# Kernel optimization log

Hardware: AMD Instinct MI355X
Metric: run time of the kernel (lower is better)

## Reference

```python
import jax, jax.numpy as jnp
import numpy as np

N, E, CN, CE = 2048, 8192, 256, 256
MN, ME = 16384, 65536
RATIO = 0.5
K_KEEP = int(np.ceil(RATIO * N))  # 1024, static


def _glorot(key, shape):
    lim = float(np.sqrt(6.0 / (shape[0] + shape[1])))
    return jax.random.uniform(key, shape, jnp.float32, -lim, lim)


def setup_inputs() -> dict:
    key = jax.random.key(0)
    ks = jax.random.split(key, 16)
    return {
        "x_n": jax.random.normal(ks[0], (N, CN), jnp.float32),
        "edge_index_n": jax.random.randint(ks[1], (2, MN), 0, N),
        "edge_weight_n": jax.random.uniform(ks[2], (MN,), jnp.float32),
        "x_e": jax.random.normal(ks[3], (E, CE), jnp.float32),
        "edge_index_e": jax.random.randint(ks[4], (2, ME), 0, E),
        "edge_weight_e": jax.random.uniform(ks[5], (ME,), jnp.float32),
        "edge_index": jax.random.randint(ks[6], (2, E), 0, N),
        "n_batch": jnp.zeros((N,), jnp.int64 if jax.config.jax_enable_x64 else jnp.int32),
        "e_batch": jnp.zeros((E,), jnp.int64 if jax.config.jax_enable_x64 else jnp.int32),
        "x_n0": jax.random.normal(ks[7], (N, CN), jnp.float32),
        "x_e0": jax.random.normal(ks[8], (E, CE), jnp.float32),
        # HodgeLaguerreConv(in, 1, K=2) params for node- and edge-scoring GNNs
        "W_n0": _glorot(ks[9], (CN, 1)),
        "W_n1": _glorot(ks[10], (CN, 1)),
        "b_n": jnp.zeros((1,), jnp.float32),
        "W_e0": _glorot(ks[11], (CE, 1)),
        "W_e1": _glorot(ks[12], (CE, 1)),
        "b_e": jnp.zeros((1,), jnp.float32),
    }


def _hodge_conv_k2(x, ei, ew, W0, W1, b):
    # PyG: out = lin0(T0) + lin1(T1), T0 = x, T1 = x - L@x (propagate: dst += w_e * x[src])
    n = x.shape[0]
    agg = jax.ops.segment_sum(ew[:, None] * x[ei[0]], ei[1], num_segments=n)
    return x @ W0 + (x - agg) @ W1 + b


def reference(x_n, edge_index_n, edge_weight_n, x_e, edge_index_e, edge_weight_e,
              edge_index, n_batch, e_batch, x_n0, x_e0,
              W_n0, W_n1, b_n, W_e0, W_e1, b_e):
    score_n = jax.nn.sigmoid(_hodge_conv_k2(x_n, edge_index_n, edge_weight_n, W_n0, W_n1, b_n).reshape(-1))
    score_e = jax.nn.sigmoid(_hodge_conv_k2(x_e, edge_index_e, edge_weight_e, W_e0, W_e1, b_e).reshape(-1))
    xns = x_n * score_n[:, None]
    xes = x_e * score_e[:, None]
    # incidence matrix B (par1): B[src,e]=-1, B[dst,e]=+1 (duplicates summed, as torch sparse)
    src, dst = edge_index[0], edge_index[1]
    eidx = jnp.arange(E)
    par1 = jnp.zeros((N, E), x_n.dtype).at[src, eidx].add(-1.0).at[dst, eidx].add(1.0)
    par1_abs = jnp.zeros((N, E), x_n.dtype).at[src, eidx].add(1.0).at[dst, eidx].add(1.0)
    # joint node score with 0.125 * |B| @ score_e
    joint = score_n + 0.125 * (par1_abs @ score_e)
    perm = jnp.argsort(-joint)                # descending
    idx_keep = jnp.sort(perm[:K_KEEP])        # kept nodes in original order (boolean-mask order)
    mask_n = jnp.zeros((N,), x_n.dtype).at[idx_keep].set(1.0)
    # edges touching any removed node get nonzero; keep edges where this is exactly 0
    removed_hits = par1_abs.T @ (1.0 - mask_n)
    keep_e = (removed_hits == 0.0).astype(x_n.dtype)     # [E]
    # masked incidence: kept-node rows, removed-edge columns zeroed
    par_masked = par1[idx_keep] * keep_e[None, :]        # [k, E]
    L0 = par_masked @ par_masked.T                       # [k, k]  (equals compacted L0)
    L1 = par_masked.T @ par_masked                       # [E, E]  (zero rows/cols at removed edges)
    # eigsh(L0, k=1, 'LM'): max eigenvalue; scipy path is non-differentiable -> stop_gradient
    lam = jax.lax.stop_gradient(jnp.linalg.eigvalsh(L0)[-1])
    L0s = 2.0 * L0 / lam
    L1s = 2.0 * L1 / lam
    x_n_out = xns[idx_keep]
    x_e_out = xes * keep_e[:, None]
    x_n0_out = x_n0[idx_keep]
    x_e0_out = x_e0 * keep_e[:, None]
    return (x_n_out, L0s, x_e_out, L1s, par_masked, x_n0_out, x_e0_out)
```

## Files before the change

kernel.cpp:

```cpp
#include <hip/hip_runtime.h>
#include <math.h>

#define NN   2048
#define EE   8192
#define CNF  256
#define MN   16384
#define ME   65536
#define KK   1024

#define OUT_XN   ((size_t)0)
#define OUT_L0   ((size_t)262144)
#define OUT_XE   ((size_t)1310720)
#define OUT_L1   ((size_t)3407872)
#define OUT_PM   ((size_t)70516736)
#define OUT_XN0  ((size_t)78905344)
#define OUT_XE0  ((size_t)79167488)

#define WS_T1N    0
#define WS_SLINN  2048
#define WS_T1E    4096
#define WS_SLINE  12288
#define WS_SCN    20480
#define WS_SCE    22528
#define WS_AGGN   32768
#define WS_AGGE   34816
#define WS_LAM    43008
#define WS_IDXK   43520
#define WS_RANK   44544
#define WS_OFFS   47616
#define WS_ADJE   66176
#define WS_KEEPE  82560

#define DCAP  8
#define PWR_T 64
#define RBAD  0xFFFFu

typedef float vf4 __attribute__((ext_vector_type(4)));

__global__ void k_prep(const float* __restrict__ xn, const float* __restrict__ xe,
                       const float* __restrict__ Wn0, const float* __restrict__ Wn1,
                       const float* __restrict__ We0, const float* __restrict__ We1,
                       float* __restrict__ wsf) {
    if (blockIdx.x == 0) {
        for (int i = threadIdx.x; i < 2048; i += 256) wsf[WS_AGGN + i] = 0.f;
        for (int i = threadIdx.x; i < 8192; i += 256) wsf[WS_AGGE + i] = 0.f;
    }
    int gw = (blockIdx.x * blockDim.x + threadIdx.x) >> 6;
    int lane = threadIdx.x & 63;
    int wstr = (gridDim.x * blockDim.x) >> 6;
    for (int row = gw; row < NN + EE; row += wstr) {
        const float *x, *W0, *W1; float *t1, *sl; int r;
        if (row < NN) { r = row;      x = xn + (size_t)r * CNF; W0 = Wn0; W1 = Wn1; t1 = wsf + WS_T1N; sl = wsf + WS_SLINN; }
        else          { r = row - NN; x = xe + (size_t)r * CNF; W0 = We0; W1 = We1; t1 = wsf + WS_T1E; sl = wsf + WS_SLINE; }
        float4 xv = ((const float4*)x)[lane];
        float4 w0 = ((const float4*)W0)[lane];
        float4 w1 = ((const float4*)W1)[lane];
        float d0 = xv.x*w0.x + xv.y*w0.y + xv.z*w0.z + xv.w*w0.w;
        float d1 = xv.x*w1.x + xv.y*w1.y + xv.z*w1.z + xv.w*w1.w;
        #pragma unroll
        for (int o = 32; o > 0; o >>= 1) { d0 += __shfl_down(d0, o, 64); d1 += __shfl_down(d1, o, 64); }
        if (lane == 0) { t1[r] = d1; sl[r] = d0 + d1; }
    }
}

__global__ void k_agg(const int* __restrict__ ein, const float* __restrict__ ewn,
                      const int* __restrict__ eie, const float* __restrict__ ewe,
                      float* __restrict__ wsf) {
    int i = blockIdx.x * blockDim.x + threadIdx.x;
    if (i < MN) {
        int s = ein[i], d = ein[MN + i];
        atomicAdd(wsf + WS_AGGN + d, ewn[i] * wsf[WS_T1N + s]);
    }
    if (i < ME) {
        int s = eie[i], d = eie[ME + i];
        atomicAdd(wsf + WS_AGGE + d, ewe[i] * wsf[WS_T1E + s]);
    }
}

__device__ __forceinline__ float block_reduce_sum(float val, float* red) {
    #pragma unroll
    for (int o = 32; o > 0; o >>= 1) val += __shfl_down(val, o, 64);
    int lane = threadIdx.x & 63, wid = threadIdx.x >> 6;
    if (lane == 0) red[wid] = val;
    __syncthreads();
    float r = 0.0f;
    if (threadIdx.x < 16) {
        r = red[threadIdx.x];
        #pragma unroll
        for (int o = 8; o > 0; o >>= 1) r += __shfl_down(r, o, 16);
        if (threadIdx.x == 0) red[0] = r;
    }
    __syncthreads();
    float out = red[0];
    __syncthreads();
    return out;
}

__global__ __launch_bounds__(1024) void k_mid(
        const int* __restrict__ ei,
        const float* __restrict__ bn, const float* __restrict__ be,
        float* __restrict__ out, float* __restrict__ wsf, int* __restrict__ wsi) {
    int tid = threadIdx.x;
    if (blockIdx.x != 0) {
        size_t w = (size_t)(blockIdx.x - 1) * 1024 + tid;
        size_t ws = (size_t)(gridDim.x - 1) * 1024;
        vf4 z = (vf4)(0.0f);
        vf4* l1 = (vf4*)(out + OUT_L1);
        for (size_t p = w; p < (size_t)EE * EE / 4; p += ws) __builtin_nontemporal_store(z, &l1[p]);
        vf4* pm = (vf4*)(out + OUT_PM);
        for (size_t p = w; p < (size_t)KK * EE / 4; p += ws) __builtin_nontemporal_store(z, &pm[p]);
        vf4* l0 = (vf4*)(out + OUT_L0);
        for (size_t p = w; p < (size_t)KK * KK / 4; p += ws) __builtin_nontemporal_store(z, &l0[p]);
        return;
    }
    __shared__ unsigned long long s_u64[2048];
    __shared__ float s_joint[2048];
    __shared__ unsigned short s_rank[2048];
    __shared__ unsigned short s_adjo[16384 + DCAP];
    __shared__ float s_red[16];
    int* s_i = (int*)s_u64;

    float bnv = bn[0], bev = be[0];
    for (int i = tid; i < NN; i += 1024) {
        float zv = wsf[WS_SLINN + i] - wsf[WS_AGGN + i] + bnv;
        float s = 1.0f / (1.0f + expf(-zv));
        wsf[WS_SCN + i] = s;
        s_joint[i] = s;
    }
    for (int j = tid; j < EE; j += 1024) {
        float zv = wsf[WS_SLINE + j] - wsf[WS_AGGE + j] + bev;
        wsf[WS_SCE + j] = 1.0f / (1.0f + expf(-zv));
    }
    __syncthreads();

    for (int e = tid; e < EE; e += 1024) {
        float v = 0.125f * wsf[WS_SCE + e];
        atomicAdd(&s_joint[ei[e]], v);
        atomicAdd(&s_joint[ei[EE + e]], v);
    }
    __syncthreads();

    for (int i = tid; i < 2048; i += 1024) {
        float f = s_joint[i];
        unsigned u = __float_as_uint(f);
        unsigned sk = (u & 0x80000000u) ? ~u : (u | 0x80000000u);
        s_u64[i] = (((unsigned long long)(~sk)) << 32) | (unsigned)i;
    }
    __syncthreads();
    for (int k = 2; k <= 2048; k <<= 1) {
        for (int j = k >> 1; j >= 1; j >>= 1) {
            for (int i = tid; i < 2048; i += 1024) {
                int ixj = i ^ j;
                if (ixj > i) {
                    bool up = ((i & k) == 0);
                    unsigned long long a = s_u64[i], b = s_u64[ixj];
                    if ((a > b) == up) { s_u64[i] = b; s_u64[ixj] = a; }
                }
            }
            __syncthreads();
        }
    }
    int myid = (int)(s_u64[tid] & 0xFFFFFFFFu);
    __syncthreads();
    {
        s_i[tid] = 0; s_i[tid + 1024] = 0; s_i[tid + 2048] = 0;
        __syncthreads();
        s_i[myid] = 1;
        __syncthreads();
        int a0 = s_i[2 * tid], a1 = s_i[2 * tid + 1];
        int pairsum = a0 + a1;
        s_i[2048 + tid] = pairsum;
        __syncthreads();
        for (int off = 1; off < 1024; off <<= 1) {
            int v = (tid >= off) ? s_i[2048 + tid - off] : 0;
            __syncthreads();
            s_i[2048 + tid] += v;
            __syncthreads();
        }
        int excl = s_i[2048 + tid] - pairsum;
        int i0 = 2 * tid, i1 = 2 * tid + 1;
        int r0 = excl, r1 = excl + a0;
        s_rank[i0] = a0 ? (unsigned short)r0 : (unsigned short)RBAD;
        s_rank[i1] = a1 ? (unsigned short)r1 : (unsigned short)RBAD;
        wsi[WS_RANK + i0] = a0 ? r0 : -1;
        wsi[WS_RANK + i1] = a1 ? r1 : -1;
        if (a0) wsi[WS_IDXK + r0] = i0;
        if (a1) wsi[WS_IDXK + r1] = i1;
    }
    __syncthreads();

    s_i[tid] = 0;
    __syncthreads();
    for (int e = tid; e < EE; e += 1024) {
        int s = ei[e], d = ei[EE + e];
        unsigned rs = s_rank[s], rd = s_rank[d];
        int kept = (rs != RBAD && rd != RBAD);
        wsi[WS_KEEPE + e] = kept;
        if (kept && s != d) {
            atomicAdd(&s_i[(int)rs], 1);
            atomicAdd(&s_i[(int)rd], 1);
        }
    }
    __syncthreads();

    {
        int dg = s_i[tid];
        s_i[1024 + tid] = dg;
        for (int off = 1; off < 1024; off <<= 1) {
            __syncthreads();
            int v = (tid >= off) ? s_i[1024 + tid - off] : 0;
            __syncthreads();
            s_i[1024 + tid] += v;
        }
        __syncthreads();
        int offs = s_i[1024 + tid] - dg;
        s_i[2048 + tid] = offs;
        wsi[WS_OFFS + tid] = offs;
        if (tid == 1023) wsi[WS_OFFS + 1024] = s_i[1024 + 1023];
    }
    __syncthreads();

    for (int e = tid; e < EE; e += 1024) {
        int s = ei[e], d = ei[EE + e];
        unsigned rs = s_rank[s], rd = s_rank[d];
        if (rs != RBAD && rd != RBAD && s != d) {
            int p = atomicAdd(&s_i[2048 + (int)rs], 1);
            s_adjo[p] = (unsigned short)rd;
            wsi[WS_ADJE + p] = (e << 1);
            int q = atomicAdd(&s_i[2048 + (int)rd], 1);
            s_adjo[q] = (unsigned short)rs;
            wsi[WS_ADJE + q] = (e << 1) | 1;
        }
    }
    __syncthreads();

    {
        int o0 = wsi[WS_OFFS + tid];
        int d  = wsi[WS_OFFS + tid + 1] - o0;
        __syncthreads();
        float* v0 = (float*)s_u64;
        float* v1 = v0 + 1024;
        unsigned h = (unsigned)tid * 2654435761u + 911u;
        h ^= h >> 15; h *= 2246822519u; h ^= h >> 13;
        v0[tid] = (float)(h & 0xFFFFu) * (1.0f / 65536.0f) - 0.5f;
        int aj[DCAP];
        #pragma unroll
        for (int j = 0; j < DCAP; ++j) aj[j] = (j < d) ? (int)s_adjo[o0 + j] : 0;
        __syncthreads();
        float* vc = v0; float* vn = v1;
        for (int iter = 0; iter < PWR_T; ++iter) {
            float acc = 0.0f;
            #pragma unroll
            for (int j = 0; j < DCAP; ++j) acc += (j < d) ? vc[aj[j]] : 0.0f;
            for (int i = o0 + DCAP; i < o0 + d; ++i) acc += vc[(int)s_adjo[i]];
            float y = (float)d * vc[tid] - acc;
            if ((iter & 7) == 7) {
                float n2 = block_reduce_sum(y * y, s_red);
                y *= (n2 > 0.0f) ? rsqrtf(n2) : 0.0f;
            }
            vn[tid] = y;
            __syncthreads();
            float* tmp = vc; vc = vn; vn = tmp;
        }
        float acc = 0.0f;
        #pragma unroll
        for (int j = 0; j < DCAP; ++j) acc += (j < d) ? vc[aj[j]] : 0.0f;
        for (int i = o0 + DCAP; i < o0 + d; ++i) acc += vc[(int)s_adjo[i]];
        float y = (float)d * vc[tid] - acc;
        float rq = block_reduce_sum(vc[tid] * y, s_red);
        if (tid == 0) wsf[WS_LAM] = rq;
    }
}

__global__ __launch_bounds__(1024) void k_final(
        const float* __restrict__ xn, const float* __restrict__ xe,
        const float* __restrict__ xn0, const float* __restrict__ xe0,
        const int* __restrict__ ei,
        float* __restrict__ out, const float* __restrict__ wsf,
        const int* __restrict__ wsi) {
    float sc = 2.0f / wsf[WS_LAM];
    int gt = blockIdx.x * 1024 + threadIdx.x;
    int gstr = gridDim.x * 1024;

    for (int i = gt; i < KK * 64; i += gstr) {
        int r = i >> 6, c = i & 63;
        int src = wsi[WS_IDXK + r];
        float s = wsf[WS_SCN + src];
        float4 v = ((const float4*)(xn + (size_t)src * CNF))[c];
        v.x *= s; v.y *= s; v.z *= s; v.w *= s;
        ((float4*)(out + OUT_XN))[(size_t)r * 64 + c] = v;
        ((float4*)(out + OUT_XN0))[(size_t)r * 64 + c] = ((const float4*)(xn0 + (size_t)src * CNF))[c];
    }
    for (int i = gt; i < EE * 64; i += gstr) {
        int e = i >> 6, c = i & 63;
        float m = wsi[WS_KEEPE + e] ? 1.0f : 0.0f;
        float s = m * wsf[WS_SCE + e];
        float4 v = ((const float4*)(xe + (size_t)e * CNF))[c];
        v.x *= s; v.y *= s; v.z *= s; v.w *= s;
        ((float4*)(out + OUT_XE))[(size_t)e * 64 + c] = v;
        float4 v0 = ((const float4*)(xe0 + (size_t)e * CNF))[c];
        v0.x *= m; v0.y *= m; v0.z *= m; v0.w *= m;
        ((float4*)(out + OUT_XE0))[(size_t)e * 64 + c] = v0;
    }
    {
        float* pm = out + OUT_PM;
        float* L0 = out + OUT_L0;
        for (int e = gt; e < EE; e += gstr) {
            int s = ei[e], d = ei[EE + e];
            int rs = wsi[WS_RANK + s], rd = wsi[WS_RANK + d];
            if (rs < 0 || rd < 0 || s == d) continue;
            pm[(size_t)rs * EE + e] = -1.0f;
            pm[(size_t)rd * EE + e] =  1.0f;
            atomicAdd(&L0[(size_t)rs * KK + rs],  sc);
            atomicAdd(&L0[(size_t)rd * KK + rd],  sc);
            atomicAdd(&L0[(size_t)rs * KK + rd], -sc);
            atomicAdd(&L0[(size_t)rd * KK + rs], -sc);
        }
    }
    {
        float* L1 = out + OUT_L1;
        int gwv = gt >> 6, lane = gt & 63, wstr = gstr >> 6;
        for (int r = gwv; r < KK; r += wstr) {
            int o0 = wsi[WS_OFFS + r], o1 = wsi[WS_OFFS + r + 1];
            for (int i = o0; i < o1; ++i) {
                int eiv = wsi[WS_ADJE + i];
                int e = eiv >> 1;
                float si = (eiv & 1) ? sc : -sc;
                for (int j = o0 + lane; j < o1; j += 64) {
                    int ejv = wsi[WS_ADJE + j];
                    atomicAdd(&L1[(size_t)e * EE + (ejv >> 1)], (ejv & 1) ? si : -si);
                }
            }
        }
    }
}

extern "C" void kernel_launch(void* const* d_in, const int* in_sizes, int n_in,
                              void* d_out, int out_size, void* d_ws, size_t ws_size,
                              hipStream_t stream) {
    const float* x_n  = (const float*)d_in[0];
    const int*   ei_n = (const int*)  d_in[1];
    const float* ew_n = (const float*)d_in[2];
    const float* x_e  = (const float*)d_in[3];
    const int*   ei_e = (const int*)  d_in[4];
    const float* ew_e = (const float*)d_in[5];
    const int*   ei   = (const int*)  d_in[6];
    const float* x_n0 = (const float*)d_in[9];
    const float* x_e0 = (const float*)d_in[10];
    const float* Wn0  = (const float*)d_in[11];
    const float* Wn1  = (const float*)d_in[12];
    const float* bn   = (const float*)d_in[13];
    const float* We0  = (const float*)d_in[14];
    const float* We1  = (const float*)d_in[15];
    const float* be   = (const float*)d_in[16];

    float* out = (float*)d_out;
    float* wsf = (float*)d_ws;
    int*   wsi = (int*)d_ws;

    k_prep <<<640, 256, 0, stream>>>(x_n, x_e, Wn0, Wn1, We0, We1, wsf);
    k_agg  <<<256, 256, 0, stream>>>(ei_n, ew_n, ei_e, ew_e, wsf);
    k_mid  <<<256, 1024, 0, stream>>>(ei, bn, be, out, wsf, wsi);
    k_final<<<256, 1024, 0, stream>>>(x_n, x_e, x_n0, x_e0, ei, out, wsf, wsi);
}
```

Before: 472.6 us.

## Replace bitonic sort with radix select, wave-scan, and single-wave power iteration

Replaces the 2048-element bitonic sort used for top-K with a 6-pass 8-bit radix select that finds the K-th key threshold, then ranks kept nodes with a shuffle-based block scan. The Hillis-Steele shared-memory scans are swapped for a wave-shuffle scan. The power iteration now runs on a single 64-lane wavefront that handles 16 nodes per lane, so it needs no block barriers, and normalisation is deferred into the next iteration. The aim is to remove the many __syncthreads in this serial block, at the cost of less parallelism in the power iteration. The Rayleigh quotient is now divided by the last norm, and tie-breaking changes to index-reversed keys.

Result: slower. 1.150 ms (+143.4%).

```diff
diff --git a/kernel.cpp b/kernel.cpp
--- a/kernel.cpp
+++ b/kernel.cpp
@@ -77,23 +77,28 @@
     }
 }
 
-__device__ __forceinline__ float block_reduce_sum(float val, float* red) {
+__device__ __forceinline__ int block_incl_scan_1024(int v, int* t16) {
+    int lane = threadIdx.x & 63, wid = threadIdx.x >> 6;
+    int x = v;
     #pragma unroll
-    for (int o = 32; o > 0; o >>= 1) val += __shfl_down(val, o, 64);
-    int lane = threadIdx.x & 63, wid = threadIdx.x >> 6;
-    if (lane == 0) red[wid] = val;
-    __syncthreads();
-    float r = 0.0f;
+    for (int o = 1; o < 64; o <<= 1) {
+        int t = __shfl_up(x, o, 64);
+        if (lane >= o) x += t;
+    }
+    if (lane == 63) t16[wid] = x;
+    __syncthreads();
     if (threadIdx.x < 16) {
-        r = red[threadIdx.x];
-        #pragma unroll
-        for (int o = 8; o > 0; o >>= 1) r += __shfl_down(r, o, 16);
-        if (threadIdx.x == 0) red[0] = r;
-    }
-    __syncthreads();
-    float out = red[0];
-    __syncthreads();
-    return out;
+        int w = t16[threadIdx.x];
+        #pragma unroll
+        for (int o = 1; o < 16; o <<= 1) {
+            int t = __shfl_up(w, o, 16);
+            if ((int)threadIdx.x >= o) w += t;
+        }
+        t16[threadIdx.x] = w;
+    }
+    __syncthreads();
+    int base = wid ? t16[wid - 1] : 0;
+    return base + x;
 }
 
 __global__ __launch_bounds__(1024) void k_mid(
@@ -117,7 +122,7 @@
     __shared__ float s_joint[2048];
     __shared__ unsigned short s_rank[2048];
     __shared__ unsigned short s_adjo[16384 + DCAP];
-    __shared__ float s_red[16];
+    __shared__ int s_t16[16];
     int* s_i = (int*)s_u64;
 
     float bnv = bn[0], bev = be[0];
@@ -140,44 +145,59 @@
     }
     __syncthreads();
 
-    for (int i = tid; i < 2048; i += 1024) {
-        float f = s_joint[i];
-        unsigned u = __float_as_uint(f);
-        unsigned sk = (u & 0x80000000u) ? ~u : (u | 0x80000000u);
-        s_u64[i] = (((unsigned long long)(~sk)) << 32) | (unsigned)i;
-    }
-    __syncthreads();
-    for (int k = 2; k <= 2048; k <<= 1) {
-        for (int j = k >> 1; j >= 1; j >>= 1) {
-            for (int i = tid; i < 2048; i += 1024) {
-                int ixj = i ^ j;
-                if (ixj > i) {
-                    bool up = ((i & k) == 0);
-                    unsigned long long a = s_u64[i], b = s_u64[ixj];
-                    if ((a > b) == up) { s_u64[i] = b; s_u64[ixj] = a; }
-                }
+    unsigned long long k0, k1;
+    {
+        int i0 = 2 * tid, i1 = 2 * tid + 1;
+        float f0 = s_joint[i0], f1 = s_joint[i1];
+        unsigned u0 = __float_as_uint(f0), u1 = __float_as_uint(f1);
+        unsigned sk0 = (u0 & 0x80000000u) ? ~u0 : (u0 | 0x80000000u);
+        unsigned sk1 = (u1 & 0x80000000u) ? ~u1 : (u1 | 0x80000000u);
+        k0 = (((unsigned long long)sk0) << 11) | (unsigned long long)(2047 - i0);
+        k1 = (((unsigned long long)sk1) << 11) | (unsigned long long)(2047 - i1);
+    }
+    unsigned long long prefix = 0ULL;
+    int rem = KK;
+    #pragma unroll
+    for (int p = 5; p >= 0; --p) {
+        __syncthreads();
+        if (tid < 256) s_i[tid] = 0;
+        __syncthreads();
+        int sh = p << 3;
+        unsigned long long ph = prefix >> (sh + 8);
+        if ((k0 >> (sh + 8)) == ph) atomicAdd(&s_i[(int)((k0 >> sh) & 255)], 1);
+        if ((k1 >> (sh + 8)) == ph) atomicAdd(&s_i[(int)((k1 >> sh) & 255)], 1);
+        __syncthreads();
+        if (tid < 64) {
+            int b0 = s_i[4 * tid + 0], b1 = s_i[4 * tid + 1];
+            int b2 = s_i[4 * tid + 2], b3 = s_i[4 * tid + 3];
+            int sl = b0 + b1 + b2 + b3;
+            int si = sl;
+            #pragma unroll
+            for (int o = 1; o < 64; o <<= 1) {
+                int t = __shfl_down(si, o, 64);
+                if (tid + o < 64) si += t;
             }
-            __syncthreads();
-        }
-    }
-    int myid = (int)(s_u64[tid] & 0xFFFFFFFFu);
-    __syncthreads();
-    {
-        s_i[tid] = 0; s_i[tid + 1024] = 0; s_i[tid + 2048] = 0;
+            int sup = si - sl;
+            int sg3 = sup;
+            int sg2 = sg3 + b3;
+            int sg1 = sg2 + b2;
+            int sg0 = sg1 + b1;
+            if (sg0 < rem && rem <= sg0 + b0) { s_i[256] = (tid << 2) | 0; s_i[257] = rem - sg0; }
+            if (sg1 < rem && rem <= sg1 + b1) { s_i[256] = (tid << 2) | 1; s_i[257] = rem - sg1; }
+            if (sg2 < rem && rem <= sg2 + b2) { s_i[256] = (tid << 2) | 2; s_i[257] = rem - sg2; }
+            if (sg3 < rem && rem <= sg3 + b3) { s_i[256] = (tid << 2) | 3; s_i[257] = rem - sg3; }
+        }
         __syncthreads();
-        s_i[myid] = 1;
+        prefix |= ((unsigned long long)(unsigned)s_i[256]) << sh;
+        rem = s_i[257];
+    }
+    {
+        int a0 = (k0 >= prefix) ? 1 : 0;
+        int a1 = (k1 >= prefix) ? 1 : 0;
+        int pr = a0 + a1;
         __syncthreads();
-        int a0 = s_i[2 * tid], a1 = s_i[2 * tid + 1];
-        int pairsum = a0 + a1;
-        s_i[2048 + tid] = pairsum;
-        __syncthreads();
-        for (int off = 1; off < 1024; off <<= 1) {
-            int v = (tid >= off) ? s_i[2048 + tid - off] : 0;
-            __syncthreads();
-            s_i[2048 + tid] += v;
-            __syncthreads();
-        }
-        int excl = s_i[2048 + tid] - pairsum;
+        int incl = block_incl_scan_1024(pr, s_t16);
+        int excl = incl - pr;
         int i0 = 2 * tid, i1 = 2 * tid + 1;
         int r0 = excl, r1 = excl + a0;
         s_rank[i0] = a0 ? (unsigned short)r0 : (unsigned short)RBAD;
@@ -205,18 +225,11 @@
 
     {
         int dg = s_i[tid];
-        s_i[1024 + tid] = dg;
-        for (int off = 1; off < 1024; off <<= 1) {
-            __syncthreads();
-            int v = (tid >= off) ? s_i[1024 + tid - off] : 0;
-            __syncthreads();
-            s_i[1024 + tid] += v;
-        }
-        __syncthreads();
-        int offs = s_i[1024 + tid] - dg;
+        int incl = block_incl_scan_1024(dg, s_t16);
+        int offs = incl - dg;
         s_i[2048 + tid] = offs;
         wsi[WS_OFFS + tid] = offs;
-        if (tid == 1023) wsi[WS_OFFS + 1024] = s_i[1024 + 1023];
+        if (tid == 1023) wsi[WS_OFFS + 1024] = incl;
     }
     __syncthreads();
 
@@ -234,41 +247,66 @@
     }
     __syncthreads();
 
-    {
-        int o0 = wsi[WS_OFFS + tid];
-        int d  = wsi[WS_OFFS + tid + 1] - o0;
-        __syncthreads();
+    if (tid >= 64) return;
+    {
+        int o0[16], dd[16];
+        #pragma unroll
+        for (int k = 0; k < 16; ++k) {
+            int n = (k << 6) | tid;
+            o0[k] = wsi[WS_OFFS + n];
+            dd[k] = wsi[WS_OFFS + n + 1] - o0[k];
+        }
         float* v0 = (float*)s_u64;
         float* v1 = v0 + 1024;
-        unsigned h = (unsigned)tid * 2654435761u + 911u;
-        h ^= h >> 15; h *= 2246822519u; h ^= h >> 13;
-        v0[tid] = (float)(h & 0xFFFFu) * (1.0f / 65536.0f) - 0.5f;
-        int aj[DCAP];
-        #pragma unroll
-        for (int j = 0; j < DCAP; ++j) aj[j] = (j < d) ? (int)s_adjo[o0 + j] : 0;
-        __syncthreads();
+        #pragma unroll
+        for (int k = 0; k < 16; ++k) {
+            int n = (k << 6) | tid;
+            unsigned h = (unsigned)n * 2654435761u + 911u;
+            h ^= h >> 15; h *= 2246822519u; h ^= h >> 13;
+            v0[n] = (float)(h & 0xFFFFu) * (1.0f / 65536.0f) - 0.5f;
+        }
+        asm volatile("s_waitcnt lgkmcnt(0)" ::: "memory");
+        __builtin_amdgcn_sched_barrier(0);
         float* vc = v0; float* vn = v1;
+        float pend = 1.0f, lastn2 = 1.0f;
         for (int iter = 0; iter < PWR_T; ++iter) {
+            float n2loc = 0.0f;
+            #pragma unroll
+            for (int k = 0; k < 16; ++k) {
+                int n = (k << 6) | tid;
+                float acc = 0.0f;
+                int e = o0[k], dc = dd[k];
+                for (int j = 0; j < dc; ++j) acc += vc[(int)s_adjo[e + j]];
+                float y = pend * ((float)dc * vc[n] - acc);
+                vn[n] = y;
+                n2loc += y * y;
+            }
+            if ((iter & 7) == 7) {
+                #pragma unroll
+                for (int o = 32; o > 0; o >>= 1) n2loc += __shfl_down(n2loc, o, 64);
+                float tot = __shfl(n2loc, 0, 64);
+                lastn2 = tot;
+                pend = (tot > 0.0f) ? rsqrtf(tot) : 0.0f;
+            } else {
+                pend = 1.0f;
+            }
+            asm volatile("s_waitcnt lgkmcnt(0)" ::: "memory");
+            __builtin_amdgcn_sched_barrier(0);
+            float* t = vc; vc = vn; vn = t;
+        }
+        float numloc = 0.0f;
+        #pragma unroll
+        for (int k = 0; k < 16; ++k) {
+            int n = (k << 6) | tid;
             float acc = 0.0f;
-            #pragma unroll
-            for (int j = 0; j < DCAP; ++j) acc += (j < d) ? vc[aj[j]] : 0.0f;
-            for (int i = o0 + DCAP; i < o0 + d; ++i) acc += vc[(int)s_adjo[i]];
-            float y = (float)d * vc[tid] - acc;
-            if ((iter & 7) == 7) {
-                float n2 = block_reduce_sum(y * y, s_red);
-                y *= (n2 > 0.0f) ? rsqrtf(n2) : 0.0f;
-            }
-            vn[tid] = y;
-            __syncthreads();
-            float* tmp = vc; vc = vn; vn = tmp;
-        }
-        float acc = 0.0f;
-        #pragma unroll
-        for (int j = 0; j < DCAP; ++j) acc += (j < d) ? vc[aj[j]] : 0.0f;
-        for (int i = o0 + DCAP; i < o0 + d; ++i) acc += vc[(int)s_adjo[i]];
-        float y = (float)d * vc[tid] - acc;
-        float rq = block_reduce_sum(vc[tid] * y, s_red);
-        if (tid == 0) wsf[WS_LAM] = rq;
+            int e = o0[k], dc = dd[k];
+            for (int j = 0; j < dc; ++j) acc += vc[(int)s_adjo[e + j]];
+            float y = (float)dc * vc[n] - acc;
+            numloc += vc[n] * y;
+        }
+        #pragma unroll
+        for (int o = 32; o > 0; o >>= 1) numloc += __shfl_down(numloc, o, 64);
+        if (tid == 0) wsf[WS_LAM] = (lastn2 > 0.0f) ? (numloc / lastn2) : 0.0f;
     }
 }
 
```
